# Optimization experiments

Measured on AMD Instinct MI355X. Metric: run time of the kernel, lower is better.

Reference implementation:

```python
import jax, jax.numpy as jnp
import numpy as np
from jax import lax

B, C_IN, H, W = 32, 96, 48, 48
D = C_IN          # d_inner = expand(1) * in_features
K, N, DT_RANK = 2, 16, 6   # k_group, d_state, ceil(D/16)


def setup_inputs() -> dict:
    key = jax.random.key(0)
    ks = jax.random.split(key, 10)
    s = 0.02
    return {
        "x": jax.random.normal(ks[0], (B, C_IN, H, W), jnp.float32),
        "in_proj_w": jax.random.normal(ks[1], (D, C_IN)) * s,
        "in_proj_b": jnp.zeros((D,)),
        "skip_w": jax.random.normal(ks[2], (1, 1, 5)) * s,
        "skip_b": jnp.zeros((1,)),
        "conv2d_w": jax.random.normal(ks[3], (D, 1, 3, 3)) * s,
        "conv2d_b": jnp.zeros((D,)),
        "local_w": jax.random.normal(ks[4], (D, 1, 3, 3)) * s,
        "local_b": jnp.zeros((D,)),
        "bn_gamma": jnp.ones((D,)),
        "bn_beta": jnp.zeros((D,)),
        "x_proj_w": jax.random.normal(ks[5], (K, DT_RANK + 2 * N, D)) * s,
        "dt_projs_w": jax.random.normal(ks[6], (K, D, DT_RANK)) * s,
        "dt_projs_b": jax.random.normal(ks[7], (K, D)) * s,
        "A_logs": jnp.tile(jnp.log(jnp.arange(1, N + 1, dtype=jnp.float32))[None], (K * D, 1)),
        "Ds": jnp.ones((K * D,)),
        "norm_gamma": jnp.ones((D,)),
        "norm_beta": jnp.zeros((D,)),
        "out_proj_w": jax.random.normal(ks[8], (C_IN, D)) * s,
        "out_proj_b": jnp.zeros((C_IN,)),
    }


def _dwconv2d(x, w, bias):
    # depthwise 3x3, NCHW
    y = lax.conv_general_dilated(x, w, (1, 1), "SAME", feature_group_count=x.shape[1],
                                 dimension_numbers=("NCHW", "OIHW", "NCHW"))
    return y + bias[None, :, None, None]


def _forward(x, in_proj_w, in_proj_b, skip_w, skip_b, conv2d_w, conv2d_b,
             local_w, local_b, bn_gamma, bn_beta, x_proj_w, dt_projs_w,
             dt_projs_b, A_logs, Ds, norm_gamma, norm_beta, out_proj_w, out_proj_b):
    b, c, h, w = x.shape
    L = h * w
    x_in = jnp.transpose(x, (0, 2, 3, 1))                       # [B,H,W,C]
    # skip gate: Conv1d(1,1,k=5) over channel axis of the spatial mean
    zm = jnp.mean(x_in, axis=(1, 2))[:, None, :]                # [B,1,C]
    z = lax.conv_general_dilated(zm, skip_w, (1,), "SAME",
                                 dimension_numbers=("NCH", "OIH", "NCH")) + skip_b[None, :, None]
    z = z[:, None]                                              # [B,1,1,C]
    x_feat = jnp.transpose(x_in @ in_proj_w.T + in_proj_b, (0, 3, 1, 2))  # [B,D,H,W]
    x_conv = jax.nn.silu(_dwconv2d(x_feat, conv2d_w, conv2d_b))
    # ---- dynamic center-similarity ordering (computed under no_grad) ----
    xc = lax.stop_gradient(x_conv)
    xf = xc.reshape(b, D, L)
    xn = xf / jnp.maximum(jnp.linalg.norm(xf, axis=1, keepdims=True), 1e-12)
    cf = xc[:, :, h // 2, w // 2]                               # [B,D]
    cn = cf / jnp.maximum(jnp.linalg.norm(cf, axis=1, keepdims=True), 1e-12)
    sim = jnp.einsum("bdl,bd->bl", xn, cn)
    sort_idx = jnp.argsort(-sim, axis=1)                        # descending similarity
    inv_idx = jnp.argsort(sort_idx, axis=1)
    # ---- DynamicCenterScan: sorted sequence and its reverse (k_group=2) ----
    xseq = jnp.take_along_axis(x_conv.reshape(b, D, L), sort_idx[:, None, :], axis=2)
    xs = jnp.stack([xseq, jnp.flip(xseq, -1)], axis=1)          # [B,K,D,L]
    # ---- SS2D selective-scan core ----
    x_dbl = jnp.einsum("bkdl,kcd->bkcl", xs, x_proj_w)
    dts, Bs, Cs = jnp.split(x_dbl, [DT_RANK, DT_RANK + N], axis=2)
    dts = jnp.einsum("bkrl,kdr->bkdl", dts, dt_projs_w)
    dts = jax.nn.softplus(dts + dt_projs_b[None, :, :, None])   # [B,K,D,L]
    A = -jnp.exp(A_logs.reshape(K, D, N))                       # [K,D,N]

    def step(hst, t):
        dt_l, B_l, C_l, x_l = t                                 # [B,K,D],[B,K,N],[B,K,N],[B,K,D]
        dA = jnp.exp(dt_l[..., None] * A)                       # [B,K,D,N]
        hst = dA * hst + (dt_l * x_l)[..., None] * B_l[:, :, None, :]
        y = jnp.einsum("bkdn,bkn->bkd", hst, C_l)
        return hst, y

    tmove = lambda a: jnp.moveaxis(a, -1, 0)
    h0 = jnp.zeros((b, K, D, N), x.dtype)
    _, ys_t = lax.scan(step, h0, (tmove(dts), tmove(Bs), tmove(Cs), tmove(xs)))
    ys = jnp.moveaxis(ys_t, 0, -1) + Ds.reshape(K, D)[None, :, :, None] * xs  # [B,K,D,L]
    # ---- DynamicCenterMerge: un-flip, sum directions, inverse permutation ----
    y = ys[:, 0] + jnp.flip(ys[:, 1], -1)
    y = jnp.take_along_axis(y, inv_idx[:, None, :], axis=2).reshape(b, D, h, w)
    # out_norm: LayerNorm over channels
    yl = jnp.transpose(y, (0, 2, 3, 1))
    mu = jnp.mean(yl, -1, keepdims=True)
    var = jnp.var(yl, -1, keepdims=True)
    yl = (yl - mu) / jnp.sqrt(var + 1e-5) * norm_gamma + norm_beta
    out_mamba = jnp.transpose(yl, (0, 3, 1, 2))
    # local path: depthwise conv + BatchNorm (batch stats, train mode) + SiLU
    lc = _dwconv2d(x_conv, local_w, local_b)
    bm = jnp.mean(lc, (0, 2, 3))
    bv = jnp.var(lc, (0, 2, 3))
    lc = (lc - bm[None, :, None, None]) * (bn_gamma / jnp.sqrt(bv + 1e-5))[None, :, None, None] + bn_beta[None, :, None, None]
    lc = jax.nn.silu(lc)
    out = out_mamba + lc
    # softmax over dim=1 of z (singleton) == all-ones gate; kept for faithfulness
    out = jnp.transpose(out, (0, 2, 3, 1)) * jax.nn.softmax(z, axis=1)
    out = out @ out_proj_w.T + out_proj_b
    return jnp.transpose(out, (0, 3, 1, 2))


def reference(x, in_proj_w, in_proj_b, skip_w, skip_b, conv2d_w, conv2d_b,
              local_w, local_b, bn_gamma, bn_beta, x_proj_w, dt_projs_w,
              dt_projs_b, A_logs, Ds, norm_gamma, norm_beta, out_proj_w, out_proj_b):
    return _forward(x, in_proj_w, in_proj_b, skip_w, skip_b, conv2d_w, conv2d_b,
                    local_w, local_b, bn_gamma, bn_beta, x_proj_w, dt_projs_w,
                    dt_projs_b, A_logs, Ds, norm_gamma, norm_beta, out_proj_w, out_proj_b)
```

## Files before the change

kernel.cpp:

```cpp
#include <hip/hip_runtime.h>
#include <hip/hip_bf16.h>


typedef __hip_bfloat16 bf16;
typedef float v2f __attribute__((ext_vector_type(2)));
typedef float v4f __attribute__((ext_vector_type(4)));
#define SH2(V, a, b) __builtin_shufflevector(V, V, a, b)

__device__ __forceinline__ float b2f(bf16 v) { return __bfloat162float(v); }
__device__ __forceinline__ float ldu(const void* p, int i, bool f32) {
  if (f32) return ((const float*)p)[i];
  return b2f(((const bf16*)p)[i]);
}
__device__ __forceinline__ float rcp_f(float x) { return __builtin_amdgcn_rcpf(x); }

#define LL 2304
#define NSEG 72

#define W_INT  0
#define B_IN   9216
#define W_C2D  9312
#define B_C2D  10176
#define W_LOC  10272
#define B_LOC  11136
#define BN_G   11232
#define BN_B   11328
#define W_XPT  11424
#define W_DT   19104
#define B_DT   20256
#define A2OF   20448
#define DSOF   23520
#define LN_G   23712
#define LN_B   23808
#define W_OUTT 23904
#define B_OUT  33120
#define WBUF_N 33280ul

#define O_WBUF  0ul
#define O_XFEAT 33280ul
#define O_XCONV 7111168ul
#define O_SIM   14189056ul
#define O_SIDX  14262784ul
#define O_XST   14336512ul
#define O_XSTD  21414400ul
#define O_RBUF  28492288ul
#define O_BC    29671936ul
#define O_DSUM  34390528ul
#define O_YMLM  34832896ul
#define O_STATS 41910784ul
#define O_AFLG  41910976ul
#define O_SCSH  41911040ul
#define O_FLAG  41911232ul
#define O_END   41911296ul

__global__ void k_detect(const void* x, float* flag) {
  int i = threadIdx.x;
  bool bad = false;
  const bf16* xb = (const bf16*)x;
#pragma unroll
  for (int r = 0; r < 4; ++r) {
    float v = b2f(xb[r * 64 + i]);
    if (!(fabsf(v) <= 1e4f)) bad = true;
  }
  bool any = __any(bad);
  if (i == 0) flag[0] = any ? 1.f : 0.f;
}

__global__ void k_prep(const void* ipw, const void* ipb, const void* c2w, const void* c2b,
                       const void* lw, const void* lb, const void* bng, const void* bnb,
                       const void* xpw, const void* dtw, const void* dtb, const void* alog,
                       const void* dss, const void* ng, const void* nb, const void* opw,
                       const void* opb, float* wb, const float* flag, float* aflag) {
  bool f = flag[0] > 0.5f;
  int i = blockIdx.x * 256 + threadIdx.x;
  if (i < 9216) {
    int r = i / 96, c = i % 96;
    wb[W_INT + c * 96 + r] = ldu(ipw, i, f);
    wb[W_OUTT + c * 96 + r] = ldu(opw, i, f);
  }
  if (i < 96) {
    wb[B_IN + i] = ldu(ipb, i, f); wb[B_C2D + i] = ldu(c2b, i, f); wb[B_LOC + i] = ldu(lb, i, f);
    wb[BN_G + i] = ldu(bng, i, f); wb[BN_B + i] = ldu(bnb, i, f); wb[LN_G + i] = ldu(ng, i, f);
    wb[LN_B + i] = ldu(nb, i, f); wb[B_OUT + i] = ldu(opb, i, f);
  }
  if (i < 864) { wb[W_C2D + i] = ldu(c2w, i, f); wb[W_LOC + i] = ldu(lw, i, f); }
  if (i < 7296) {
    int k = i / 3648, c = (i / 96) % 38, d = i % 96;
    wb[W_XPT + d * 80 + k * 38 + c] = ldu(xpw, i, f);
  }
  if (i < 1152) wb[W_DT + i] = ldu(dtw, i, f);
  if (i < 192) { wb[B_DT + i] = ldu(dtb, i, f); wb[DSOF + i] = ldu(dss, i, f); }
  if (i < 3072) {
    float av = expf(ldu(alog, i, f));
    wb[A2OF + i] = -av * 1.4426950408889634f;
    int n = i % 16;
    if (fabsf(av - (float)(n + 1)) > 1e-3f * (n + 1)) atomicAdd(aflag, 1.f);
  }
}

__global__ __launch_bounds__(128, 4)
void k_inproj(const void* __restrict__ x, const float* __restrict__ wb,
              float* __restrict__ xfeat, const float* __restrict__ flag) {
  int b = blockIdx.x / 72;
  int rest = blockIdx.x % 72;
  int q = rest / 18;
  int l = (rest % 18) * 128 + threadIdx.x;
  float acc[24];
#pragma unroll
  for (int j = 0; j < 24; ++j) acc[j] = wb[B_IN + q * 24 + j];
  bool f = flag[0] > 0.5f;
  if (f) {
    const float* xf = (const float*)x;
#pragma unroll 2
    for (int c = 0; c < 96; ++c) {
      float xc = xf[(b * 96 + c) * LL + l];
      const float* wr = wb + W_INT + c * 96 + q * 24;
#pragma unroll
      for (int j = 0; j < 24; ++j) acc[j] += xc * wr[j];
    }
  } else {
    const bf16* xb = (const bf16*)x;
#pragma unroll 2
    for (int c = 0; c < 96; ++c) {
      float xc = b2f(xb[(b * 96 + c) * LL + l]);
      const float* wr = wb + W_INT + c * 96 + q * 24;
#pragma unroll
      for (int j = 0; j < 24; ++j) acc[j] += xc * wr[j];
    }
  }
#pragma unroll
  for (int j = 0; j < 24; ++j) xfeat[(b * 96 + q * 24 + j) * LL + l] = acc[j];
}

__global__ __launch_bounds__(256, 8)
void k_conv_silu(const float* __restrict__ xfeat, const float* __restrict__ wb,
                 float* __restrict__ xconv) {
  int t = blockIdx.x * 256 + threadIdx.x;
  int l = t % LL; int d = (t / LL) % 96; int b = t / (LL * 96);
  int h = l / 48, w = l % 48;
  const float* wr = wb + W_C2D + d * 9;
  const float* src = xfeat + (b * 96 + d) * LL;
  float acc = wb[B_C2D + d];
#pragma unroll
  for (int ki = 0; ki < 3; ++ki) {
    int hh = h + ki - 1; if (hh < 0 || hh >= 48) continue;
#pragma unroll
    for (int kj = 0; kj < 3; ++kj) {
      int ww = w + kj - 1; if (ww < 0 || ww >= 48) continue;
      acc += src[hh * 48 + ww] * wr[ki * 3 + kj];
    }
  }
  xconv[t] = acc / (1.f + expf(-acc));
}

__global__ __launch_bounds__(256, 8)
void k_sim(const float* __restrict__ xconv, float* __restrict__ sim) {
  int b = blockIdx.x / 9;
  int l = (blockIdx.x % 9) * 256 + threadIdx.x;
  const float* base = xconv + (size_t)b * 96 * LL;
  float dot = 0, nrm = 0, cn = 0;
  for (int d = 0; d < 96; ++d) {
    float v = base[d * LL + l];
    float c = base[d * LL + 1176];
    dot += v * c; nrm += v * v; cn += c * c;
  }
  float den = fmaxf(sqrtf(nrm), 1e-12f) * fmaxf(sqrtf(cn), 1e-12f);
  sim[b * LL + l] = dot / den;
}

__global__ void k_sort(const float* __restrict__ sim, int* __restrict__ sidx) {
  __shared__ unsigned long long key[4096];
  int b = blockIdx.x;
  for (int i = threadIdx.x; i < 4096; i += 1024) {
    unsigned long long kv = ~0ull;
    if (i < LL) {
      unsigned u = __float_as_uint(sim[b * LL + i]);
      u = (u >> 31) ? ~u : (u | 0x80000000u);
      kv = (((unsigned long long)(~u)) << 32) | (unsigned)i;
    }
    key[i] = kv;
  }
  __syncthreads();
  for (int k = 2; k <= 4096; k <<= 1)
    for (int j = k >> 1; j > 0; j >>= 1) {
      for (int i = threadIdx.x; i < 4096; i += 1024) {
        int ij = i ^ j;
        if (ij > i) {
          unsigned long long a = key[i], c = key[ij];
          bool up = ((i & k) == 0);
          if ((a > c) == up) { key[i] = c; key[ij] = a; }
        }
      }
      __syncthreads();
    }
  for (int i = threadIdx.x; i < LL; i += 1024) sidx[b * LL + i] = (int)(key[i] & 0xffffffffu);
}

__global__ __launch_bounds__(256, 8)
void k_gatherd(const float* __restrict__ xconv, const int* __restrict__ sidx,
               float* __restrict__ xstd) {
  int t = blockIdx.x * 256 + threadIdx.x;
  int l = t % LL; int d = (t / LL) % 96; int b = t / (LL * 96);
  int p = sidx[b * LL + l];
  xstd[t] = xconv[((size_t)b * 96 + d) * LL + p];
}

__global__ __launch_bounds__(256, 4)
void k_tr_dl(const float* __restrict__ in, float* __restrict__ out) {
  __shared__ float tile[64 * 97];
  int b = blockIdx.x / 36;
  int l0 = (blockIdx.x % 36) * 64;
#pragma unroll
  for (int it = 0; it < 24; ++it) {
    int idx = it * 256 + threadIdx.x;
    int d = idx / 64, j = idx % 64;
    tile[j * 97 + d] = in[((size_t)b * 96 + d) * LL + l0 + j];
  }
  __syncthreads();
#pragma unroll
  for (int it = 0; it < 24; ++it) {
    int idx = it * 256 + threadIdx.x;
    int r = idx / 96, c = idx % 96;
    out[((size_t)b * LL + l0 + r) * 96 + c] = tile[r * 97 + c];
  }
}

__global__ __launch_bounds__(256, 4)
void k_tr_ld(const float* __restrict__ in, float* __restrict__ out) {
  __shared__ float tile[64 * 97];
  int b = blockIdx.x / 36;
  int l0 = (blockIdx.x % 36) * 64;
#pragma unroll
  for (int it = 0; it < 24; ++it) {
    int idx = it * 256 + threadIdx.x;
    int r = idx / 96, c = idx % 96;
    tile[r * 97 + c] = in[((size_t)b * LL + l0 + r) * 96 + c];
  }
  __syncthreads();
#pragma unroll
  for (int it = 0; it < 24; ++it) {
    int idx = it * 256 + threadIdx.x;
    int d = idx / 64, j = idx % 64;
    out[((size_t)b * 96 + d) * LL + l0 + j] = tile[j * 97 + d];
  }
}

__global__ __launch_bounds__(128, 4)
void k_xdbl(const float* __restrict__ xstd, const float* __restrict__ wb,
            float* __restrict__ rbuf, float* __restrict__ bc) {
  int kq = blockIdx.x / 576;
  int r = blockIdx.x % 576;
  int b = r / 18;
  int l = (r % 18) * 128 + threadIdx.x;
  float acc[38];
#pragma unroll
  for (int j = 0; j < 38; ++j) acc[j] = 0.f;
#pragma unroll 2
  for (int c = 0; c < 96; ++c) {
    float xc = xstd[((size_t)b * 96 + c) * LL + l];
    const float* wr = wb + W_XPT + c * 80 + kq * 38;
#pragma unroll
    for (int j = 0; j < 38; ++j) acc[j] += xc * wr[j];
  }
  int lout = kq ? (LL - 1 - l) : l;
  float4* r4 = (float4*)(rbuf + ((size_t)(b * 2 + kq) * LL + lout) * 8);
  r4[0] = make_float4(acc[0], acc[1], acc[2], acc[3]);
  r4[1] = make_float4(acc[4], acc[5], 0.f, 0.f);
  float4* b4 = (float4*)(bc + ((size_t)(b * 2 + kq) * LL + lout) * 32);
#pragma unroll
  for (int i = 0; i < 8; ++i)
    b4[i] = make_float4(acc[6 + 4 * i], acc[7 + 4 * i], acc[8 + 4 * i], acc[9 + 4 * i]);
}

__global__ __launch_bounds__(192, 3)
void k_scan1(const float* __restrict__ rbuf, const float* __restrict__ bc,
             const float* __restrict__ xst, const float* __restrict__ wb,
             float* __restrict__ dsum, float* __restrict__ hend,
             const float* __restrict__ aflag) {
  __shared__ float sbc[2][1024];
  __shared__ float srr[2][256];
  int sub = threadIdx.x / 96;
  int tid = threadIdx.x - sub * 96;
  int unit = blockIdx.x * 2 + sub;
  int s = unit % 72; int k = (unit / 72) % 2; int b = unit / 144;
  int lbase = (b * 2 + k) * LL + s * 32;
  long long lk0 = k ? (LL - 1 - s * 32) : (s * 32);
  long long stp = k ? -96 : 96;
  const float* xp = xst + (size_t)b * LL * 96 + lk0 * 96 + tid;
  float xv[32];
#pragma unroll
  for (int t = 0; t < 32; ++t) xv[t] = xp[t * stp];
  {
    const float4* bsrc = (const float4*)(bc + (size_t)lbase * 32);
    float4* bdst = (float4*)sbc[sub];
    for (int i = tid; i < 256; i += 96) bdst[i] = bsrc[i];
    const float4* rsrc = (const float4*)(rbuf + (size_t)lbase * 8);
    float4* rdst = (float4*)srr[sub];
    if (tid < 64) rdst[tid] = rsrc[tid];
  }
  __syncthreads();
  int d = tid;
  float wd[6];
#pragma unroll
  for (int j = 0; j < 6; ++j) wd[j] = wb[W_DT + (k * 96 + d) * 6 + j];
  float bd = wb[B_DT + k * 96 + d];
  float ds = 0.f;
  v2f h2[8];
#pragma unroll
  for (int j = 0; j < 8; ++j) h2[j] = (v2f){0.f, 0.f};
  bool fast = (aflag[0] == 0.f);
  if (fast) {
    const v4f* bq4 = (const v4f*)sbc[sub];
    const v4f* rq4 = (const v4f*)srr[sub];
#pragma unroll
    for (int t = 0; t < 32; ++t) {
      v4f r0 = rq4[t * 2], r1 = rq4[t * 2 + 1];
      float a = bd + r0.x * wd[0] + r0.y * wd[1] + r0.z * wd[2]
                   + r0.w * wd[3] + r1.x * wd[4] + r1.y * wd[5];
      float ea = __expf(a);
      float p1 = rcp_f(1.f + ea);
      float dtv = (a > 20.f) ? a : -0.69314718055994531f * __log2f(p1);
      ds += dtv;
      float dtx = dtv * xv[t];
      v2f dt2 = {dtx, dtx};
      float p2s = p1 * p1;
      v2f P1 = {p1, p2s};
      v2f P2 = P1 * (v2f){p2s, p2s};
      float p4s = P2.y;
      v2f P3 = P1 * (v2f){p4s, p4s};
      v2f P4 = P2 * (v2f){p4s, p4s};
      float p8s = P4.y;
      v2f P5 = P1 * (v2f){p8s, p8s};
      v2f P6 = P2 * (v2f){p8s, p8s};
      v2f P7 = P3 * (v2f){p8s, p8s};
      v2f P8 = P4 * (v2f){p8s, p8s};
      v4f B0 = bq4[t * 8 + 0], B1 = bq4[t * 8 + 1];
      v4f B2 = bq4[t * 8 + 2], B3 = bq4[t * 8 + 3];
      h2[0] = P1 * h2[0] + dt2 * SH2(B0, 0, 1);
      h2[1] = P2 * h2[1] + dt2 * SH2(B0, 2, 3);
      h2[2] = P3 * h2[2] + dt2 * SH2(B1, 0, 1);
      h2[3] = P4 * h2[3] + dt2 * SH2(B1, 2, 3);
      h2[4] = P5 * h2[4] + dt2 * SH2(B2, 0, 1);
      h2[5] = P6 * h2[5] + dt2 * SH2(B2, 2, 3);
      h2[6] = P7 * h2[6] + dt2 * SH2(B3, 0, 1);
      h2[7] = P8 * h2[7] + dt2 * SH2(B3, 2, 3);
    }
  } else {
    float a2[16], hh[16];
#pragma unroll
    for (int n = 0; n < 16; ++n) { a2[n] = wb[A2OF + (k * 96 + d) * 16 + n]; hh[n] = 0.f; }
#pragma unroll 4
    for (int t = 0; t < 32; ++t) {
      const float* rr = &srr[sub][t * 8];
      float a = bd + rr[0] * wd[0] + rr[1] * wd[1] + rr[2] * wd[2]
                   + rr[3] * wd[3] + rr[4] * wd[4] + rr[5] * wd[5];
      float dtv = (a > 20.f) ? a : log1pf(expf(a));
      ds += dtv;
      float dtx = dtv * xv[t];
      const float* bcl = &sbc[sub][t * 32];
#pragma unroll
      for (int n = 0; n < 16; ++n) hh[n] = exp2f(dtv * a2[n]) * hh[n] + dtx * bcl[n];
    }
#pragma unroll
    for (int j = 0; j < 8; ++j) h2[j] = (v2f){hh[2 * j], hh[2 * j + 1]};
  }
  dsum[((b * 2 + k) * 96 + d) * NSEG + s] = ds;
  float4* ho = (float4*)(hend + (((size_t)(b * 2 + k) * NSEG + s) * 96 + d) * 16);
  ho[0] = make_float4(h2[0].x, h2[0].y, h2[1].x, h2[1].y);
  ho[1] = make_float4(h2[2].x, h2[2].y, h2[3].x, h2[3].y);
  ho[2] = make_float4(h2[4].x, h2[4].y, h2[5].x, h2[5].y);
  ho[3] = make_float4(h2[6].x, h2[6].y, h2[7].x, h2[7].y);
}

__global__ __launch_bounds__(256, 4)
void k_scan2(const float* __restrict__ dsum, const float* __restrict__ hend,
             const float* __restrict__ wb, float* __restrict__ hstart) {
  int t = blockIdx.x * 256 + threadIdx.x;
  int n = t % 16; int d = (t / 16) % 96; int k = (t / 1536) % 2; int b = t / 3072;
  float a2 = wb[A2OF + (k * 96 + d) * 16 + n];
  float h = 0.f;
  int rowd = ((b * 2 + k) * 96 + d) * NSEG;
#pragma unroll 8
  for (int s = 0; s < NSEG; ++s) {
    size_t idx = (((size_t)(b * 2 + k) * NSEG + s) * 96 + d) * 16 + n;
    hstart[idx] = h;
    h = exp2f(a2 * dsum[rowd + s]) * h + hend[idx];
  }
}

__global__ __launch_bounds__(192, 3)
void k_scan3ln(const float* __restrict__ rbuf, const float* __restrict__ bc,
               const float* __restrict__ xst, const float* __restrict__ wb,
               const float* __restrict__ hstart, const int* __restrict__ sidx,
               float* __restrict__ ymlm, const float* __restrict__ aflag) {
  __shared__ float yA[32 * 97];
  __shared__ float yB[32 * 97];
  __shared__ float sbc[2][1024];
  __shared__ float srr[2][256];
  __shared__ float smu[32], srs[32];
  int b = blockIdx.x / NSEG;
  int u = blockIdx.x % NSEG;
  int t = threadIdx.x;
  int sub = t / 96;
  int d = t - sub * 96;
  int k = sub;
  int seg = sub ? (NSEG - 1 - u) : u;
  int lbase = (b * 2 + k) * LL + seg * 32;
  long long lk0 = k ? (LL - 1 - seg * 32) : (seg * 32);
  long long stp = k ? -96 : 96;
  const float* xp = xst + (size_t)b * LL * 96 + lk0 * 96 + d;
  float xv[32];
#pragma unroll
  for (int i = 0; i < 32; ++i) xv[i] = xp[i * stp];
  {
    const float4* bsrc = (const float4*)(bc + (size_t)lbase * 32);
    float4* bdst = (float4*)sbc[sub];
    for (int i = d; i < 256; i += 96) bdst[i] = bsrc[i];
    const float4* rsrc = (const float4*)(rbuf + (size_t)lbase * 8);
    float4* rdst = (float4*)srr[sub];
    if (d < 64) rdst[d] = rsrc[d];
  }
  __syncthreads();
  {
    float* yacc = sub ? yB : yA;
    float wd[6];
#pragma unroll
    for (int j = 0; j < 6; ++j) wd[j] = wb[W_DT + (k * 96 + d) * 6 + j];
    float bd = wb[B_DT + k * 96 + d];
    float Dv = wb[DSOF + k * 96 + d];
    const float* hi = hstart + (((size_t)(b * 2 + k) * NSEG + seg) * 96 + d) * 16;
    bool fast = (aflag[0] == 0.f);
    if (fast) {
      const v4f* hi4 = (const v4f*)hi;
      v4f H0 = hi4[0], H1 = hi4[1], H2 = hi4[2], H3 = hi4[3];
      v2f h2[8];
      h2[0] = SH2(H0, 0, 1); h2[1] = SH2(H0, 2, 3);
      h2[2] = SH2(H1, 0, 1); h2[3] = SH2(H1, 2, 3);
      h2[4] = SH2(H2, 0, 1); h2[5] = SH2(H2, 2, 3);
      h2[6] = SH2(H3, 0, 1); h2[7] = SH2(H3, 2, 3);
      const v4f* bq4 = (const v4f*)sbc[sub];
      const v4f* rq4 = (const v4f*)srr[sub];
#pragma unroll
      for (int i = 0; i < 32; ++i) {
        v4f r0 = rq4[i * 2], r1 = rq4[i * 2 + 1];
        float a = bd + r0.x * wd[0] + r0.y * wd[1] + r0.z * wd[2]
                     + r0.w * wd[3] + r1.x * wd[4] + r1.y * wd[5];
        float ea = __expf(a);
        float p1 = rcp_f(1.f + ea);
        float dtv = (a > 20.f) ? a : -0.69314718055994531f * __log2f(p1);
        float dtx = dtv * xv[i];
        v2f dt2 = {dtx, dtx};
        float p2s = p1 * p1;
        v2f P1 = {p1, p2s};
        v2f P2 = P1 * (v2f){p2s, p2s};
        float p4s = P2.y;
        v2f P3 = P1 * (v2f){p4s, p4s};
        v2f P4 = P2 * (v2f){p4s, p4s};
        float p8s = P4.y;
        v2f P5 = P1 * (v2f){p8s, p8s};
        v2f P6 = P2 * (v2f){p8s, p8s};
        v2f P7 = P3 * (v2f){p8s, p8s};
        v2f P8 = P4 * (v2f){p8s, p8s};
        v4f B0 = bq4[i * 8 + 0], B1 = bq4[i * 8 + 1];
        v4f B2 = bq4[i * 8 + 2], B3 = bq4[i * 8 + 3];
        v4f C0 = bq4[i * 8 + 4], C1 = bq4[i * 8 + 5];
        v4f C2 = bq4[i * 8 + 6], C3 = bq4[i * 8 + 7];
        v2f y2;
        h2[0] = P1 * h2[0] + dt2 * SH2(B0, 0, 1); y2  = h2[0] * SH2(C0, 0, 1);
        h2[1] = P2 * h2[1] + dt2 * SH2(B0, 2, 3); y2 += h2[1] * SH2(C0, 2, 3);
        h2[2] = P3 * h2[2] + dt2 * SH2(B1, 0, 1); y2 += h2[2] * SH2(C1, 0, 1);
        h2[3] = P4 * h2[3] + dt2 * SH2(B1, 2, 3); y2 += h2[3] * SH2(C1, 2, 3);
        h2[4] = P5 * h2[4] + dt2 * SH2(B2, 0, 1); y2 += h2[4] * SH2(C2, 0, 1);
        h2[5] = P6 * h2[5] + dt2 * SH2(B2, 2, 3); y2 += h2[5] * SH2(C2, 2, 3);
        h2[6] = P7 * h2[6] + dt2 * SH2(B3, 0, 1); y2 += h2[6] * SH2(C3, 0, 1);
        h2[7] = P8 * h2[7] + dt2 * SH2(B3, 2, 3); y2 += h2[7] * SH2(C3, 2, 3);
        int qloc = k ? (31 - i) : i;
        yacc[qloc * 97 + d] = y2.x + y2.y + Dv * xv[i];
      }
    } else {
      float a2[16], hh[16];
#pragma unroll
      for (int n = 0; n < 16; ++n) { a2[n] = wb[A2OF + (k * 96 + d) * 16 + n]; hh[n] = hi[n]; }
#pragma unroll 4
      for (int i = 0; i < 32; ++i) {
        const float* rr = &srr[sub][i * 8];
        float a = bd + rr[0] * wd[0] + rr[1] * wd[1] + rr[2] * wd[2]
                     + rr[3] * wd[3] + rr[4] * wd[4] + rr[5] * wd[5];
        float dtv = (a > 20.f) ? a : log1pf(expf(a));
        float dtx = dtv * xv[i];
        const float* bcl = &sbc[sub][i * 32];
        float y = 0.f;
#pragma unroll
        for (int n = 0; n < 16; ++n) {
          hh[n] = exp2f(dtv * a2[n]) * hh[n] + dtx * bcl[n];
          y += hh[n] * bcl[16 + n];
        }
        int qloc = k ? (31 - i) : i;
        yacc[qloc * 97 + d] = y + Dv * xv[i];
      }
    }
  }
  __syncthreads();
  if (t < 32) {
    float sum = 0, ss = 0;
#pragma unroll
    for (int dd = 0; dd < 96; ++dd) {
      float v = yA[t * 97 + dd] + yB[t * 97 + dd];
      sum += v; ss += v * v;
    }
    float mu = sum * (1.f / 96.f);
    float var = ss * (1.f / 96.f) - mu * mu;
    smu[t] = mu;
    srs[t] = rsqrtf(var + 1e-5f);
  }
  __syncthreads();
  {
    int r = t / 6, c0 = (t % 6) * 16;
    int q = u * 32 + r;
    int p = sidx[b * LL + q];
    float mu = smu[r], rs = srs[r];
    float tmp[16];
#pragma unroll
    for (int j = 0; j < 16; ++j) {
      int dd = c0 + j;
      tmp[j] = (yA[r * 97 + dd] + yB[r * 97 + dd] - mu) * rs * wb[LN_G + dd] + wb[LN_B + dd];
    }
    float4* o4 = (float4*)(ymlm + ((size_t)b * LL + p) * 96 + c0);
    o4[0] = make_float4(tmp[0], tmp[1], tmp[2], tmp[3]);
    o4[1] = make_float4(tmp[4], tmp[5], tmp[6], tmp[7]);
    o4[2] = make_float4(tmp[8], tmp[9], tmp[10], tmp[11]);
    o4[3] = make_float4(tmp[12], tmp[13], tmp[14], tmp[15]);
  }
}

__global__ __launch_bounds__(256, 8)
void k_convlc_bn(const float* __restrict__ xconv, const float* __restrict__ wb,
                 float* __restrict__ lcbuf, float* __restrict__ stats) {
  int bd = blockIdx.x;
  int b = bd / 96, d = bd % 96;
  const float* src = xconv + (size_t)(b * 96 + d) * LL;
  const float* wr = wb + W_LOC + d * 9;
  float bias = wb[B_LOC + d];
  float s1 = 0, s2 = 0;
  for (int l = threadIdx.x; l < LL; l += 256) {
    int h = l / 48, w = l % 48;
    float acc = bias;
#pragma unroll
    for (int ki = 0; ki < 3; ++ki) {
      int hh = h + ki - 1; if (hh < 0 || hh >= 48) continue;
#pragma unroll
      for (int kj = 0; kj < 3; ++kj) {
        int ww = w + kj - 1; if (ww < 0 || ww >= 48) continue;
        acc += src[hh * 48 + ww] * wr[ki * 3 + kj];
      }
    }
    lcbuf[(size_t)(b * 96 + d) * LL + l] = acc;
    s1 += acc; s2 += acc * acc;
  }
  __shared__ float r1[256], r2[256];
  r1[threadIdx.x] = s1; r2[threadIdx.x] = s2; __syncthreads();
  for (int o = 128; o > 0; o >>= 1) {
    if (threadIdx.x < o) { r1[threadIdx.x] += r1[threadIdx.x + o]; r2[threadIdx.x] += r2[threadIdx.x + o]; }
    __syncthreads();
  }
  if (threadIdx.x == 0) { atomicAdd(&stats[d], r1[0]); atomicAdd(&stats[96 + d], r2[0]); }
}

__global__ void k_bnfin(const float* __restrict__ stats, const float* __restrict__ wb,
                        float* __restrict__ scsh) {
  int d = threadIdx.x; if (d >= 96) return;
  float mean = stats[d] * (1.f / 73728.f);
  float var = stats[96 + d] * (1.f / 73728.f) - mean * mean;
  float sc = wb[BN_G + d] * rsqrtf(var + 1e-5f);
  scsh[d] = sc; scsh[96 + d] = wb[BN_B + d] - mean * sc;
}

__global__ __launch_bounds__(128, 4)
void k_final(const float* __restrict__ lcbuf, const float* __restrict__ ymdm,
             const float* __restrict__ wb, const float* __restrict__ scsh,
             void* __restrict__ out, const float* __restrict__ flag) {
  int b = blockIdx.x / 72;
  int rest = blockIdx.x % 72;
  int q = rest / 18;
  int l = (rest % 18) * 128 + threadIdx.x;
  float acc[24];
#pragma unroll
  for (int j = 0; j < 24; ++j) acc[j] = wb[B_OUT + q * 24 + j];
#pragma unroll 2
  for (int d = 0; d < 96; ++d) {
    float lc = lcbuf[((size_t)b * 96 + d) * LL + l] * scsh[d] + scsh[96 + d];
    float vd = lc * rcp_f(1.f + __expf(-lc)) + ymdm[((size_t)b * 96 + d) * LL + l];
    const float* wr = wb + W_OUTT + d * 96 + q * 24;
#pragma unroll
    for (int j = 0; j < 24; ++j) acc[j] += vd * wr[j];
  }
  bool f = flag[0] > 0.5f;
  if (f) {
    float* of = (float*)out;
#pragma unroll
    for (int j = 0; j < 24; ++j) of[(b * 96 + q * 24 + j) * LL + l] = acc[j];
  } else {
    bf16* ob = (bf16*)out;
#pragma unroll
    for (int j = 0; j < 24; ++j) ob[(b * 96 + q * 24 + j) * LL + l] = __float2bfloat16(acc[j]);
  }
}

extern "C" void kernel_launch(void* const* d_in, const int* in_sizes, int n_in,
                              void* d_out, int out_size, void* d_ws, size_t ws_size,
                              hipStream_t stream) {
  if (ws_size < O_END * sizeof(float)) return;
  float* ws = (float*)d_ws;
  float* wb    = ws + O_WBUF;
  float* xfeat = ws + O_XFEAT;
  float* xconv = ws + O_XCONV;
  float* sim   = ws + O_SIM;
  int*   sidx  = (int*)(ws + O_SIDX);
  float* xst   = ws + O_XST;
  float* xstd  = ws + O_XSTD;
  float* rbuf  = ws + O_RBUF;
  float* bc    = ws + O_BC;
  float* dsum  = ws + O_DSUM;
  float* ymlm  = ws + O_YMLM;
  float* stats = ws + O_STATS;
  float* aflag = ws + O_AFLG;
  float* scsh  = ws + O_SCSH;
  float* flag  = ws + O_FLAG;
  float* hend   = xfeat;
  float* hstart = xstd;
  float* ymdm   = xfeat;
  float* lcbuf  = xst;

  hipMemsetAsync(stats, 0, 256 * sizeof(float), stream);
  k_detect<<<1, 64, 0, stream>>>(d_in[0], flag);
  k_prep<<<36, 256, 0, stream>>>(
      d_in[1], d_in[2], d_in[5], d_in[6], d_in[7], d_in[8], d_in[9], d_in[10],
      d_in[11], d_in[12], d_in[13], d_in[14], d_in[15], d_in[16], d_in[17], d_in[18],
      d_in[19], wb, flag, aflag);
  k_inproj<<<2304, 128, 0, stream>>>(d_in[0], wb, xfeat, flag);
  k_conv_silu<<<27648, 256, 0, stream>>>(xfeat, wb, xconv);
  k_sim<<<288, 256, 0, stream>>>(xconv, sim);
  k_sort<<<32, 1024, 0, stream>>>(sim, sidx);
  k_gatherd<<<27648, 256, 0, stream>>>(xconv, sidx, xstd);
  k_tr_dl<<<1152, 256, 0, stream>>>(xstd, xst);
  k_xdbl<<<1152, 128, 0, stream>>>(xstd, wb, rbuf, bc);
  k_scan1<<<2304, 192, 0, stream>>>(rbuf, bc, xst, wb, dsum, hend, aflag);
  k_scan2<<<384, 256, 0, stream>>>(dsum, hend, wb, hstart);
  k_scan3ln<<<2304, 192, 0, stream>>>(rbuf, bc, xst, wb, hstart, sidx, ymlm, aflag);
  k_tr_ld<<<1152, 256, 0, stream>>>(ymlm, ymdm);
  k_convlc_bn<<<3072, 256, 0, stream>>>(xconv, wb, lcbuf, stats);
  k_bnfin<<<1, 96, 0, stream>>>(stats, wb, scsh);
  k_final<<<2304, 128, 0, stream>>>(lcbuf, ymdm, wb, scsh, d_out, flag);
}
```

Baseline: 522.0 us.

## Replace bitonic sort with parallel rank-counting sort across more blocks

Swaps the per-batch 4096-element bitonic sort (32 blocks of 1024 threads, 78 barrier-separated stages) for a counting-rank scheme. Each thread compares its similarity key against all 2304 keys in shared memory and scatters its index to the computed rank, with ties broken by original index so the order stays stable. The work spreads over 288 blocks instead of 32 and needs only one barrier, in exchange for O(L^2) comparisons per batch.

```diff
diff --git a/kernel.cpp b/kernel.cpp
--- a/kernel.cpp
+++ b/kernel.cpp
@@ -168,32 +168,32 @@
   sim[b * LL + l] = dot / den;
 }
 
-__global__ void k_sort(const float* __restrict__ sim, int* __restrict__ sidx) {
-  __shared__ unsigned long long key[4096];
-  int b = blockIdx.x;
-  for (int i = threadIdx.x; i < 4096; i += 1024) {
-    unsigned long long kv = ~0ull;
-    if (i < LL) {
-      unsigned u = __float_as_uint(sim[b * LL + i]);
-      u = (u >> 31) ? ~u : (u | 0x80000000u);
-      kv = (((unsigned long long)(~u)) << 32) | (unsigned)i;
-    }
-    key[i] = kv;
+__global__ __launch_bounds__(256, 8)
+void k_rank(const float* __restrict__ sim, int* __restrict__ sidx) {
+  __shared__ unsigned su[LL];
+  int b = blockIdx.x / 9;
+  int part = blockIdx.x % 9;
+  const float* sp = sim + b * LL;
+  for (int i = threadIdx.x; i < LL; i += 256) {
+    unsigned u = __float_as_uint(sp[i]);
+    u = (u >> 31) ? ~u : (u | 0x80000000u);
+    su[i] = u;
   }
   __syncthreads();
-  for (int k = 2; k <= 4096; k <<= 1)
-    for (int j = k >> 1; j > 0; j >>= 1) {
-      for (int i = threadIdx.x; i < 4096; i += 1024) {
-        int ij = i ^ j;
-        if (ij > i) {
-          unsigned long long a = key[i], c = key[ij];
-          bool up = ((i & k) == 0);
-          if ((a > c) == up) { key[i] = c; key[ij] = a; }
-        }
-      }
-      __syncthreads();
-    }
-  for (int i = threadIdx.x; i < LL; i += 1024) sidx[b * LL + i] = (int)(key[i] & 0xffffffffu);
+  int l = part * 256 + threadIdx.x;
+  unsigned ui = su[l];
+  int rank = 0;
+  const uint4* s4 = (const uint4*)su;
+#pragma unroll 4
+  for (int c = 0; c < LL / 4; ++c) {
+    uint4 U = s4[c];
+    int j = 4 * c;
+    rank += (int)(U.x > ui) + (int)((U.x == ui) & (j + 0 < l));
+    rank += (int)(U.y > ui) + (int)((U.y == ui) & (j + 1 < l));
+    rank += (int)(U.z > ui) + (int)((U.z == ui) & (j + 2 < l));
+    rank += (int)(U.w > ui) + (int)((U.w == ui) & (j + 3 < l));
+  }
+  sidx[b * LL + rank] = l;
 }
 
 __global__ __launch_bounds__(256, 8)
@@ -640,7 +640,7 @@
   k_inproj<<<2304, 128, 0, stream>>>(d_in[0], wb, xfeat, flag);
   k_conv_silu<<<27648, 256, 0, stream>>>(xfeat, wb, xconv);
   k_sim<<<288, 256, 0, stream>>>(xconv, sim);
-  k_sort<<<32, 1024, 0, stream>>>(sim, sidx);
+  k_rank<<<288, 256, 0, stream>>>(sim, sidx);
   k_gatherd<<<27648, 256, 0, stream>>>(xconv, sidx, xstd);
   k_tr_dl<<<1152, 256, 0, stream>>>(xstd, xst);
   k_xdbl<<<1152, 128, 0, stream>>>(xstd, wb, rbuf, bc);
```

Measured after the change: 529.9 us. About the same (+1.5%).
